# Optimization experiments

Measured on AMD Instinct MI355X. Metric: run time of the kernel, lower is better.

Reference implementation:

```python
import jax, jax.numpy as jnp
import numpy as np

N, T, D_MODEL, H, DK = 4, 4096, 1024, 16, 64


def setup_inputs() -> dict:
    key = jax.random.key(0)
    ks = jax.random.split(key, 16)
    randn = lambda k, sh: jax.random.normal(k, sh, dtype=jnp.float32)
    # linear weights stored (in, out) so y = x @ W + b (math-equivalent to torch Linear)
    scale = 1.0 / np.sqrt(D_MODEL)
    return {
        "x_k": randn(ks[0], (N, T, D_MODEL)),
        "x_v": randn(ks[1], (N, T, D_MODEL)),
        "x_q": randn(ks[2], (N, T, D_MODEL)),
        "mask": jnp.ones((N, T), dtype=jnp.int32),
        "Wk": randn(ks[3], (D_MODEL, H * DK)) * scale,
        "bk": randn(ks[4], (H * DK,)) * 0.02,
        "Wv": randn(ks[5], (D_MODEL, H * DK)) * scale,
        "bv": randn(ks[6], (H * DK,)) * 0.02,
        "Wq": randn(ks[7], (D_MODEL, H * DK)) * scale,
        "bq": randn(ks[8], (H * DK,)) * 0.02,
        "alpha_w": randn(ks[9], (DK,)),
        "beta_w": randn(ks[10], (DK,)),
        "Wr": randn(ks[11], (DK, DK)) * (1.0 / np.sqrt(DK)),
        "br": randn(ks[12], (DK,)) * 0.02,
        "Wfc": randn(ks[13], (H * DK, D_MODEL)) * scale,
        "bfc": randn(ks[14], (D_MODEL,)) * 0.02,
    }


def _split_heads(x):  # (n, t, h*d) -> (n, h, t, d)
    n, t, _ = x.shape
    return x.reshape(n, t, H, DK).transpose(0, 2, 1, 3)


def reference(x_k, x_v, x_q, mask, Wk, bk, Wv, bv, Wq, bq,
              alpha_w, beta_w, Wr, br, Wfc, bfc):
    scale = DK ** (-0.5)
    k = _split_heads(x_k @ Wk + bk)  # (n, h, t, d)
    v = _split_heads(x_v @ Wv + bv)
    q = _split_heads(x_q @ Wq + bq)

    m = (mask == 0)[:, None, :]  # (n, 1, t) True where masked
    neg_inf = jnp.finfo(q.dtype).min

    # alpha pooling over queries -> global query (n, h, d)
    alpha = jnp.einsum('nhtd,d->nht', q, alpha_w) * scale
    alpha = jnp.where(m, neg_inf, alpha)
    alpha = jax.nn.softmax(alpha, axis=-1)
    global_query = jnp.einsum('nht,nhtd->nhd', alpha, q)

    # p = broadcast(global_query) * k, then beta pooling -> global key
    p = global_query[:, :, None, :] * k  # (n, h, t, d)
    beta = jnp.einsum('nhtd,d->nht', p, beta_w) * scale
    beta = jnp.where(m, neg_inf, beta)
    beta = jax.nn.softmax(beta, axis=-1)
    global_key = jnp.einsum('nht,nhtd->nhd', beta, p)

    u = global_key[:, :, None, :] * v  # (n, h, t, d)
    u_r = u @ Wr + br
    A = u_r + q  # (n, h, t, d)
    A = A.transpose(0, 2, 1, 3).reshape(N, T, H * DK)
    return A @ Wfc + bfc
```

## Files before the change

kernel.cpp:

```cpp
#include <hip/hip_runtime.h>

typedef __bf16 bf16x8 __attribute__((ext_vector_type(8)));
typedef float f32x4 __attribute__((ext_vector_type(4)));
typedef unsigned int u32x4 __attribute__((ext_vector_type(4)));
typedef unsigned short u16x4 __attribute__((ext_vector_type(4)));
typedef unsigned short u16x8 __attribute__((ext_vector_type(8)));

#define SEQ_T 4096
#define DMODEL 1024
#define HEADS 16
#define DKH 64
#define MTOK 16384

#define AS1 __attribute__((address_space(1)))
#define AS3 __attribute__((address_space(3)))
#define MEMFENCE asm volatile("" ::: "memory")

__device__ __forceinline__ unsigned short f2bf(float f) {
  unsigned u = __builtin_bit_cast(unsigned int, f);
  u += 0x7FFFu + ((u >> 16) & 1u);
  return (unsigned short)(u >> 16);
}
__device__ __forceinline__ float bf2f(unsigned short h) {
  unsigned u = ((unsigned)h) << 16;
  return __builtin_bit_cast(float, u);
}
__device__ __forceinline__ void gload16(const unsigned short* g, unsigned short* l) {
  __builtin_amdgcn_global_load_lds((const AS1 unsigned int*)(g),
                                   (AS3 unsigned int*)(l), 16, 0, 0);
}

__global__ void __launch_bounds__(256) k_wtrans(const float* __restrict__ W,
                                                unsigned short* __restrict__ Wt,
                                                int K, int N) {
  __shared__ float tile[32][33];
  int bn = blockIdx.x * 32, bk = blockIdx.y * 32;
  int tx = threadIdx.x, ty = threadIdx.y;
#pragma unroll
  for (int j = 0; j < 32; j += 8)
    tile[ty + j][tx] = W[(size_t)(bk + ty + j) * N + bn + tx];
  __syncthreads();
#pragma unroll
  for (int j = 0; j < 32; j += 8)
    Wt[(size_t)(bn + ty + j) * K + bk + tx] = f2bf(tile[tx][ty + j]);
}

#define BM 128
#define BN 128
#define BK 64

template <int OBF, int SCORE, int AF32>
__global__ void __launch_bounds__(256, 2)
k_gemm(const void* __restrict__ Ain, const unsigned short* __restrict__ Bt,
       const float* __restrict__ bias, void* __restrict__ C,
       const int* __restrict__ mask, const float* __restrict__ swt,
       float* __restrict__ sbuf, int M, int N, int K) {
  __shared__ unsigned short As[BM * BK];
  __shared__ unsigned short Bs[BN * BK];
  const int tid = threadIdx.x;
  const int lane = tid & 63, wid = tid >> 6;
  const int wr = wid >> 1, wc = wid & 1;
  const int l15 = lane & 15, l4 = lane >> 4;

  const int nwg = gridDim.x * gridDim.y;
  const int flat = blockIdx.x + blockIdx.y * gridDim.x;
  const int rm = (flat & 7) * (nwg >> 3) + (flat >> 3);
  const int bx = rm % gridDim.x, by = rm / gridDim.x;
  const int bm = by * BM, bn = bx * BN;

  const float* Af = (const float*)Ain;
  const unsigned short* Abf = (const unsigned short*)Ain;
  const int nt = K / BK;

  f32x4 acc[4][4];
#pragma unroll
  for (int i = 0; i < 4; ++i)
#pragma unroll
    for (int j = 0; j < 4; ++j)
#pragma unroll
      for (int e = 0; e < 4; ++e) acc[i][j][e] = 0.f;

  const int sgr = lane >> 3;
  const int sgc = (lane & 7) ^ sgr;
  const int r0 = tid >> 2;
  const int c4 = tid & 3;
  f32x4 alv[2][4];

  auto stageB = [&](int t) {
#pragma unroll
    for (int j = 0; j < 4; ++j) {
      int g = wid * 4 + j;
      gload16(Bt + (size_t)(bn + g * 8 + sgr) * K + t * BK + sgc * 8,
              Bs + g * 512);
    }
  };
  auto stageAbf = [&](int t) {
#pragma unroll
    for (int j = 0; j < 4; ++j) {
      int g = wid * 4 + j;
      gload16(Abf + (size_t)(bm + g * 8 + sgr) * K + t * BK + sgc * 8,
              As + g * 512);
    }
  };
  auto aload = [&](int t) {
#pragma unroll
    for (int s = 0; s < 2; ++s) {
      const float* src = Af + (size_t)(bm + r0 + s * 64) * K + t * BK + c4 * 16;
#pragma unroll
      for (int j = 0; j < 4; ++j) alv[s][j] = *(const f32x4*)(src + j * 4);
    }
  };
  auto awrite = [&]() {
#pragma unroll
    for (int s = 0; s < 2; ++s) {
      int row = r0 + s * 64;
#pragma unroll
      for (int half = 0; half < 2; ++half) {
        u16x8 o;
#pragma unroll
        for (int j = 0; j < 8; ++j) o[j] = f2bf(alv[s][half * 2 + (j >> 2)][j & 3]);
        int ch = (c4 * 2 + half) ^ (row & 7);
        *(u16x8*)(As + row * BK + ch * 8) = o;
      }
    }
  };

  if (AF32) aload(0);

  for (int t = 0; t < nt; ++t) {
    __syncthreads();
    if (AF32) awrite();
    else stageAbf(t);
    stageB(t);
    __syncthreads();
#pragma unroll
    for (int kh = 0; kh < 2; ++kh) {
      bf16x8 af[4], bfr[4];
#pragma unroll
      for (int m = 0; m < 4; ++m) {
        int ra = wr * 64 + m * 16 + l15;
        int c7 = (kh * 4 + l4) ^ (ra & 7);
        af[m] = *(const bf16x8*)(As + ra * BK + c7 * 8);
      }
#pragma unroll
      for (int n = 0; n < 4; ++n) {
        int rb = wc * 64 + n * 16 + l15;
        int c7 = (kh * 4 + l4) ^ (rb & 7);
        bfr[n] = *(const bf16x8*)(Bs + rb * BK + c7 * 8);
      }
      if (AF32 && kh == 0 && t + 1 < nt) aload(t + 1);
#pragma unroll
      for (int m = 0; m < 4; ++m)
#pragma unroll
        for (int n = 0; n < 4; ++n)
          acc[m][n] = __builtin_amdgcn_mfma_f32_16x16x32_bf16(af[m], bfr[n],
                                                              acc[m][n], 0, 0, 0);
    }
  }

  const int crow = bm + wr * 64 + l4 * 4;
  const int ccol = bn + wc * 64 + l15;
  float pacc[4][4];
  const float* wrow = nullptr;
  if (SCORE == 1) wrow = swt;
  if (SCORE == 2) wrow = swt + ((size_t)((bm >> 12) * HEADS + bx * 2 + wc)) * DKH;
  if (SCORE) {
#pragma unroll
    for (int m = 0; m < 4; ++m)
#pragma unroll
      for (int e = 0; e < 4; ++e) pacc[m][e] = 0.f;
  }

#pragma unroll
  for (int m = 0; m < 4; ++m)
#pragma unroll
    for (int n = 0; n < 4; ++n) {
      int c = ccol + n * 16;
      float bj = bias[c];
      float wg = SCORE ? wrow[n * 16 + l15] : 0.f;
#pragma unroll
      for (int e = 0; e < 4; ++e) {
        int r = crow + m * 16 + e;
        float v = acc[m][n][e] + bj;
        if (SCORE) pacc[m][e] += v * wg;
        if (OBF)
          ((unsigned short*)C)[(size_t)r * N + c] = f2bf(v);
        else
          ((float*)C)[(size_t)r * N + c] = v;
      }
    }

  if (SCORE) {
#pragma unroll
    for (int m = 0; m < 4; ++m)
#pragma unroll
      for (int e = 0; e < 4; ++e) {
        float p = pacc[m][e];
        p += __shfl_xor(p, 1);
        p += __shfl_xor(p, 2);
        p += __shfl_xor(p, 4);
        p += __shfl_xor(p, 8);
        if (l15 == 0) {
          int r = crow + m * 16 + e;
          int tt = r & (SEQ_T - 1), n = r >> 12;
          float sc = p * 0.125f;
          if (mask[n * SEQ_T + tt] == 0) sc = -3.0e38f;
          sbuf[((size_t)n * HEADS + bx * 2 + wc) * SEQ_T + tt] = sc;
        }
      }
  }
}

__global__ void __launch_bounds__(256) k_stat1(const float* __restrict__ s,
                                               float* __restrict__ pmax,
                                               float* __restrict__ psum) {
  __shared__ float red[4];
  const int b = blockIdx.x, tid = threadIdx.x, lane = tid & 63, wid = tid >> 6;
  float v = s[(size_t)b * 256 + tid];
  float m = v;
#pragma unroll
  for (int o = 1; o < 64; o <<= 1) m = fmaxf(m, __shfl_xor(m, o));
  if (lane == 0) red[wid] = m;
  __syncthreads();
  m = fmaxf(fmaxf(red[0], red[1]), fmaxf(red[2], red[3]));
  __syncthreads();
  float e = __expf(v - m);
#pragma unroll
  for (int o = 1; o < 64; o <<= 1) e += __shfl_xor(e, o);
  if (lane == 0) red[wid] = e;
  __syncthreads();
  if (tid == 0) {
    pmax[b] = m;
    psum[b] = red[0] + red[1] + red[2] + red[3];
  }
}

__global__ void __launch_bounds__(64) k_stat2(const float* __restrict__ pmax,
                                              const float* __restrict__ psum,
                                              float* __restrict__ smx,
                                              float* __restrict__ sinv) {
  const int b = blockIdx.x, lane = threadIdx.x;
  float pm = -3.4e38f, ps = 0.f;
  if (lane < 16) {
    pm = pmax[b * 16 + lane];
    ps = psum[b * 16 + lane];
  }
  float gm = pm;
#pragma unroll
  for (int o = 1; o < 16; o <<= 1) gm = fmaxf(gm, __shfl_xor(gm, o));
  float sc = ps * __expf(pm - gm);
#pragma unroll
  for (int o = 1; o < 16; o <<= 1) sc += __shfl_xor(sc, o);
  if (lane == 0) {
    smx[b] = gm;
    sinv[b] = 1.f / sc;
  }
}

__global__ void __launch_bounds__(256) k_wsum(const unsigned short* __restrict__ X,
                                              const float* __restrict__ s,
                                              const float* __restrict__ mxv,
                                              const float* __restrict__ invv,
                                              float* __restrict__ pbuf) {
  __shared__ float part[16][64];
  const int nh = blockIdx.x >> 4, chunk = blockIdx.x & 15;
  const int n = nh >> 4, h = nh & 15;
  const int tid = threadIdx.x, lane = tid & 63, wid = tid >> 6;
  const int tsub = lane >> 4, dl = lane & 15;
  const float mx = mxv[nh], inv = invv[nh];
  const float* sb = s + (size_t)nh * SEQ_T + chunk * 256;
  const size_t base = ((size_t)n * SEQ_T + chunk * 256) * DMODEL + h * DKH + dl * 4;
  f32x4 acc = {0.f, 0.f, 0.f, 0.f};
  for (int t = wid * 4 + tsub; t < 256; t += 16) {
    float w = __expf(sb[t] - mx) * inv;
    u16x4 xv = *(const u16x4*)(X + base + (size_t)t * DMODEL);
    acc[0] += w * bf2f(xv[0]);
    acc[1] += w * bf2f(xv[1]);
    acc[2] += w * bf2f(xv[2]);
    acc[3] += w * bf2f(xv[3]);
  }
  int g = wid * 4 + tsub;
#pragma unroll
  for (int e = 0; e < 4; ++e) part[g][dl * 4 + e] = acc[e];
  __syncthreads();
  if (tid < 64) {
    float v = 0.f;
#pragma unroll
    for (int gg = 0; gg < 16; ++gg) v += part[gg][tid];
    pbuf[(size_t)blockIdx.x * 64 + tid] = v;
  }
}

template <int MODE>
__global__ void __launch_bounds__(64) k_fin(const float* __restrict__ pbuf,
                                            const float* __restrict__ gq,
                                            const float* __restrict__ bw,
                                            float* __restrict__ out,
                                            float* __restrict__ wv) {
  const int nh = blockIdx.x, d = threadIdx.x;
  float v = 0.f;
#pragma unroll
  for (int c = 0; c < 16; ++c) v += pbuf[((size_t)nh * 16 + c) * 64 + d];
  if (MODE == 1) v *= gq[(size_t)nh * 64 + d];
  out[(size_t)nh * 64 + d] = v;
  if (MODE == 0) wv[(size_t)nh * 64 + d] = v * bw[d];
}

__global__ void __launch_bounds__(256) k_wrg(const float* __restrict__ gk,
                                             const float* __restrict__ Wr,
                                             unsigned short* __restrict__ WrgT) {
  const int nh = blockIdx.x, tid = threadIdx.x;
#pragma unroll
  for (int i = 0; i < 16; ++i) {
    int idx = i * 256 + tid;
    int d = idx >> 6, dd = idx & 63;
    WrgT[(size_t)nh * 4096 + idx] = f2bf(gk[nh * 64 + dd] * Wr[dd * 64 + d]);
  }
}

#define ABM 128
#define VLD 72
__global__ void __launch_bounds__(256) k_abuild2(const unsigned short* __restrict__ v,
                                                 const unsigned short* __restrict__ qbf,
                                                 const unsigned short* __restrict__ WrgT,
                                                 const float* __restrict__ br,
                                                 unsigned short* __restrict__ A) {
  __shared__ unsigned short Vs[ABM * VLD];
  __shared__ unsigned short Ws[DKH * VLD];
  const int tid = threadIdx.x, lane = tid & 63, wid = tid >> 6;
  const int nh = blockIdx.y;
  const int n = nh >> 4, h = nh & 15;
  const size_t nt0 = (size_t)n * SEQ_T + (size_t)blockIdx.x * ABM;
  const size_t vbase = nt0 * DMODEL + (size_t)h * DKH;
#pragma unroll
  for (int p = 0; p < 4; ++p) {
    int idx = p * 256 + tid;
    int row = idx >> 3, c = idx & 7;
    *(u32x4*)(Vs + row * VLD + c * 8) =
        *(const u32x4*)(v + vbase + (size_t)row * DMODEL + c * 8);
  }
#pragma unroll
  for (int p = 0; p < 2; ++p) {
    int idx = p * 256 + tid;
    int row = idx >> 3, c = idx & 7;
    *(u32x4*)(Ws + row * VLD + c * 8) =
        *(const u32x4*)(WrgT + (size_t)nh * 4096 + row * 64 + c * 8);
  }
  __syncthreads();
  const int l15 = lane & 15, l4 = lane >> 4;
  f32x4 acc[2][4];
#pragma unroll
  for (int m = 0; m < 2; ++m)
#pragma unroll
    for (int nf = 0; nf < 4; ++nf)
#pragma unroll
      for (int e = 0; e < 4; ++e) acc[m][nf][e] = 0.f;
#pragma unroll
  for (int ks = 0; ks < 2; ++ks) {
    bf16x8 af[2], bfr[4];
#pragma unroll
    for (int m = 0; m < 2; ++m)
      af[m] = *(const bf16x8*)(Vs + (wid * 32 + m * 16 + l15) * VLD + l4 * 8 + ks * 32);
#pragma unroll
    for (int nf = 0; nf < 4; ++nf)
      bfr[nf] = *(const bf16x8*)(Ws + (nf * 16 + l15) * VLD + l4 * 8 + ks * 32);
#pragma unroll
    for (int m = 0; m < 2; ++m)
#pragma unroll
      for (int nf = 0; nf < 4; ++nf)
        acc[m][nf] = __builtin_amdgcn_mfma_f32_16x16x32_bf16(af[m], bfr[nf],
                                                             acc[m][nf], 0, 0, 0);
  }
#pragma unroll
  for (int m = 0; m < 2; ++m)
#pragma unroll
    for (int nf = 0; nf < 4; ++nf) {
      int d = nf * 16 + l15;
      float bj = br[d];
#pragma unroll
      for (int e = 0; e < 4; ++e) {
        int r = wid * 32 + m * 16 + l4 * 4 + e;
        size_t off = vbase + (size_t)r * DMODEL + d;
        float val = acc[m][nf][e] + bj + bf2f(qbf[off]);
        A[off] = f2bf(val);
      }
    }
}

extern "C" void kernel_launch(void* const* d_in, const int* in_sizes, int n_in,
                              void* d_out, int out_size, void* d_ws, size_t ws_size,
                              hipStream_t stream) {
  const float* x_k = (const float*)d_in[0];
  const float* x_v = (const float*)d_in[1];
  const float* x_q = (const float*)d_in[2];
  const int* mask = (const int*)d_in[3];
  const float* Wk = (const float*)d_in[4];
  const float* bk = (const float*)d_in[5];
  const float* Wv = (const float*)d_in[6];
  const float* bv = (const float*)d_in[7];
  const float* Wq = (const float*)d_in[8];
  const float* bq = (const float*)d_in[9];
  const float* alpha_w = (const float*)d_in[10];
  const float* beta_w = (const float*)d_in[11];
  const float* Wr = (const float*)d_in[12];
  const float* br = (const float*)d_in[13];
  const float* Wfc = (const float*)d_in[14];
  const float* bfc = (const float*)d_in[15];

  unsigned short* qbf = (unsigned short*)d_out;

  char* ws = (char*)d_ws;
  const size_t SZ_XBF = (size_t)MTOK * DMODEL * 2;
  unsigned short* kbf = (unsigned short*)(ws);
  unsigned short* vbf = (unsigned short*)(ws + SZ_XBF);
  unsigned short* xst = (unsigned short*)(ws + 2 * SZ_XBF);
  unsigned short* WkT = (unsigned short*)(ws + 3 * SZ_XBF);
  unsigned short* WvT = WkT + (size_t)DMODEL * DMODEL;
  unsigned short* WqT = WvT + (size_t)DMODEL * DMODEL;
  unsigned short* WfT = WqT + (size_t)DMODEL * DMODEL;
  unsigned short* WrgT = WfT + (size_t)DMODEL * DMODEL;
  float* gq = (float*)(WrgT + (size_t)64 * 4096);
  float* gk = gq + 4096;
  float* wvb = gk + 4096;
  float* sbuf = wvb + 4096;
  float* pbuf = sbuf + (size_t)64 * SEQ_T;
  float* pmax = pbuf + 1024 * 64;
  float* psum = pmax + 1024;
  float* smx = psum + 1024;
  float* sinv = smx + 64;

  dim3 tb(32, 8);
  dim3 tg(DMODEL / 32, DMODEL / 32);
  k_wtrans<<<tg, tb, 0, stream>>>(Wq, WqT, DMODEL, DMODEL);
  k_wtrans<<<tg, tb, 0, stream>>>(Wk, WkT, DMODEL, DMODEL);
  k_wtrans<<<tg, tb, 0, stream>>>(Wv, WvT, DMODEL, DMODEL);
  k_wtrans<<<tg, tb, 0, stream>>>(Wfc, WfT, DMODEL, DMODEL);

  dim3 ggrid(DMODEL / BN, MTOK / BM);

  k_gemm<1, 1, 1><<<ggrid, 256, 0, stream>>>(x_q, WqT, bq, (void*)qbf, mask,
                                             alpha_w, sbuf, MTOK, DMODEL, DMODEL);
  k_stat1<<<1024, 256, 0, stream>>>(sbuf, pmax, psum);
  k_stat2<<<64, 64, 0, stream>>>(pmax, psum, smx, sinv);
  k_wsum<<<1024, 256, 0, stream>>>(qbf, sbuf, smx, sinv, pbuf);
  k_fin<0><<<64, 64, 0, stream>>>(pbuf, nullptr, beta_w, gq, wvb);

  k_gemm<1, 2, 1><<<ggrid, 256, 0, stream>>>(x_k, WkT, bk, (void*)kbf, mask,
                                             wvb, sbuf, MTOK, DMODEL, DMODEL);
  k_stat1<<<1024, 256, 0, stream>>>(sbuf, pmax, psum);
  k_stat2<<<64, 64, 0, stream>>>(pmax, psum, smx, sinv);
  k_wsum<<<1024, 256, 0, stream>>>(kbf, sbuf, smx, sinv, pbuf);
  k_fin<1><<<64, 64, 0, stream>>>(pbuf, gq, nullptr, gk, nullptr);

  k_gemm<1, 0, 1><<<ggrid, 256, 0, stream>>>(x_v, WvT, bv, (void*)vbf, nullptr,
                                             nullptr, nullptr, MTOK, DMODEL, DMODEL);

  k_wrg<<<64, 256, 0, stream>>>(gk, Wr, WrgT);
  dim3 agrid(SEQ_T / ABM, 64);
  k_abuild2<<<agrid, 256, 0, stream>>>(vbf, qbf, WrgT, br, xst);

  k_gemm<0, 0, 0><<<ggrid, 256, 0, stream>>>(xst, WfT, bfc, d_out, nullptr,
                                             nullptr, nullptr, MTOK, DMODEL, DMODEL);
}
```

Before: 331.3 us.

## Restructure GEMM main loop with double-buffered A tile and manual waitcnt pipelining

Reworks the k_gemm mainloop so the fp32 A tile is double-buffered in LDS and prefetched two iterations ahead, with explicit s_waitcnt and raw s_barrier in place of __syncthreads. Each thread now loads a row-half of A. MFMA blocks are wrapped in s_setprio. Launch bounds go from 2 to 3 waves per SIMD. The aim is to overlap global loads and fp32-to-bf16 conversion with MFMA work and to cut barrier stalls. In exchange, the fp32-A path uses more LDS and more registers, the higher occupancy target may cause spills, and the hand-counted vmcnt values must be exactly right.

```diff
diff --git a/kernel.cpp b/kernel.cpp
--- a/kernel.cpp
+++ b/kernel.cpp
@@ -50,12 +50,12 @@
 #define BK 64
 
 template <int OBF, int SCORE, int AF32>
-__global__ void __launch_bounds__(256, 2)
+__global__ void __launch_bounds__(256, 3)
 k_gemm(const void* __restrict__ Ain, const unsigned short* __restrict__ Bt,
        const float* __restrict__ bias, void* __restrict__ C,
        const int* __restrict__ mask, const float* __restrict__ swt,
        float* __restrict__ sbuf, int M, int N, int K) {
-  __shared__ unsigned short As[BM * BK];
+  __shared__ unsigned short As[(AF32 ? 2 : 1) * BM * BK];
   __shared__ unsigned short Bs[BN * BK];
   const int tid = threadIdx.x;
   const int lane = tid & 63, wid = tid >> 6;
@@ -82,79 +82,101 @@
 
   const int sgr = lane >> 3;
   const int sgc = (lane & 7) ^ sgr;
-  const int r0 = tid >> 2;
-  const int c4 = tid & 3;
-  f32x4 alv[2][4];
-
+  const int r0 = tid >> 1, ahalf = tid & 1;
+  f32x4 alv[8];
+
+  auto aload = [&](int t) {
+    const float* src = Af + (size_t)(bm + r0) * K + t * BK + ahalf * 32;
+#pragma unroll
+    for (int j = 0; j < 8; ++j) alv[j] = *(const f32x4*)(src + j * 4);
+  };
+  auto awrite = [&](int t) {
+    unsigned short* dst = As + (AF32 ? (t & 1) * (BM * BK) : 0);
+#pragma unroll
+    for (int j = 0; j < 4; ++j) {
+      u16x8 o;
+#pragma unroll
+      for (int e = 0; e < 8; ++e) o[e] = f2bf(alv[2 * j + (e >> 2)][e & 3]);
+      int slot = (ahalf * 4 + j) ^ (r0 & 7);
+      *(u16x8*)(dst + r0 * BK + slot * 8) = o;
+    }
+  };
+  auto stageA = [&](int t) {
+#pragma unroll
+    for (int j = 0; j < 4; ++j) {
+      int rb = wid * 32 + j * 8;
+      gload16(Abf + (size_t)(bm + rb + sgr) * K + t * BK + sgc * 8, As + rb * BK);
+    }
+  };
   auto stageB = [&](int t) {
 #pragma unroll
     for (int j = 0; j < 4; ++j) {
-      int g = wid * 4 + j;
-      gload16(Bt + (size_t)(bn + g * 8 + sgr) * K + t * BK + sgc * 8,
-              Bs + g * 512);
+      int rb = wid * 32 + j * 8;
+      gload16(Bt + (size_t)(bn + rb + sgr) * K + t * BK + sgc * 8, Bs + rb * BK);
     }
   };
-  auto stageAbf = [&](int t) {
-#pragma unroll
-    for (int j = 0; j < 4; ++j) {
-      int g = wid * 4 + j;
-      gload16(Abf + (size_t)(bm + g * 8 + sgr) * K + t * BK + sgc * 8,
-              As + g * 512);
-    }
-  };
-  auto aload = [&](int t) {
-#pragma unroll
-    for (int s = 0; s < 2; ++s) {
-      const float* src = Af + (size_t)(bm + r0 + s * 64) * K + t * BK + c4 * 16;
-#pragma unroll
-      for (int j = 0; j < 4; ++j) alv[s][j] = *(const f32x4*)(src + j * 4);
-    }
-  };
-  auto awrite = [&]() {
-#pragma unroll
-    for (int s = 0; s < 2; ++s) {
-      int row = r0 + s * 64;
-#pragma unroll
-      for (int half = 0; half < 2; ++half) {
-        u16x8 o;
-#pragma unroll
-        for (int j = 0; j < 8; ++j) o[j] = f2bf(alv[s][half * 2 + (j >> 2)][j & 3]);
-        int ch = (c4 * 2 + half) ^ (row & 7);
-        *(u16x8*)(As + row * BK + ch * 8) = o;
-      }
-    }
-  };
-
-  if (AF32) aload(0);
+
+  if (AF32) {
+    aload(0);
+    awrite(0);
+    stageB(0);
+    if (nt > 1) aload(1);
+    asm volatile("s_waitcnt vmcnt(8) lgkmcnt(0)" ::: "memory");
+  } else {
+    stageA(0);
+    stageB(0);
+    asm volatile("s_waitcnt vmcnt(0) lgkmcnt(0)" ::: "memory");
+  }
+  __builtin_amdgcn_sched_barrier(0);
+  __builtin_amdgcn_s_barrier();
+  MEMFENCE;
 
   for (int t = 0; t < nt; ++t) {
-    __syncthreads();
-    if (AF32) awrite();
-    else stageAbf(t);
-    stageB(t);
-    __syncthreads();
+    const unsigned short* Ab = As + (AF32 ? (t & 1) * (BM * BK) : 0);
 #pragma unroll
     for (int kh = 0; kh < 2; ++kh) {
       bf16x8 af[4], bfr[4];
 #pragma unroll
       for (int m = 0; m < 4; ++m) {
         int ra = wr * 64 + m * 16 + l15;
-        int c7 = (kh * 4 + l4) ^ (ra & 7);
-        af[m] = *(const bf16x8*)(As + ra * BK + c7 * 8);
+        int sl = (kh * 4 + l4) ^ (ra & 7);
+        af[m] = *(const bf16x8*)(Ab + ra * BK + sl * 8);
       }
 #pragma unroll
       for (int n = 0; n < 4; ++n) {
-        int rb = wc * 64 + n * 16 + l15;
-        int c7 = (kh * 4 + l4) ^ (rb & 7);
-        bfr[n] = *(const bf16x8*)(Bs + rb * BK + c7 * 8);
-      }
-      if (AF32 && kh == 0 && t + 1 < nt) aload(t + 1);
+        int rb2 = wc * 64 + n * 16 + l15;
+        int sl = (kh * 4 + l4) ^ (rb2 & 7);
+        bfr[n] = *(const bf16x8*)(Bs + rb2 * BK + sl * 8);
+      }
+      __builtin_amdgcn_s_setprio(1);
 #pragma unroll
       for (int m = 0; m < 4; ++m)
 #pragma unroll
         for (int n = 0; n < 4; ++n)
           acc[m][n] = __builtin_amdgcn_mfma_f32_16x16x32_bf16(af[m], bfr[n],
                                                               acc[m][n], 0, 0, 0);
+      __builtin_amdgcn_s_setprio(0);
+    }
+    MEMFENCE;
+    __builtin_amdgcn_s_barrier();
+    MEMFENCE;
+    if (t + 1 < nt) {
+      stageB(t + 1);
+      if (AF32) {
+        awrite(t + 1);
+        if (t + 2 < nt) {
+          aload(t + 2);
+          asm volatile("s_waitcnt vmcnt(8) lgkmcnt(0)" ::: "memory");
+        } else {
+          asm volatile("s_waitcnt vmcnt(0) lgkmcnt(0)" ::: "memory");
+        }
+      } else {
+        stageA(t + 1);
+        asm volatile("s_waitcnt vmcnt(0) lgkmcnt(0)" ::: "memory");
+      }
+      __builtin_amdgcn_sched_barrier(0);
+      __builtin_amdgcn_s_barrier();
+      MEMFENCE;
     }
   }
 
```

New measurement: 396.5 us. 1.2x slower.
